# Kernel optimization log

Hardware: AMD Instinct MI355X
Metric: run time of the kernel (lower is better)

The kernel has to match this reference:

```python
import jax, jax.numpy as jnp
import numpy as np

N, E = 50000, 1600000
D_IN, D_OUT = 256, 64
ALPHA = 0.2        # LeakyReLU slope used on attention logits (self.leakyrelu)
BT_SLOPE = 0.01    # F.leaky_relu default slope inside relu_bt


def _xavier_normal(key, shape, gain):
    fan_in, fan_out = shape[0], shape[1]
    std = gain * np.sqrt(2.0 / (fan_in + fan_out))
    return jax.random.normal(key, shape, dtype=jnp.float32) * std


def relu_bt(x):
    # -threshold(-leaky_relu(x), -t, -t) == min(leaky_relu(x), t), t = ||x||_inf (detached)
    t = jax.lax.stop_gradient(jnp.max(jnp.abs(x)))
    y = jnp.where(x >= 0, x, BT_SLOPE * x)
    return jnp.minimum(y, t)


def setup_inputs() -> dict:
    key = jax.random.key(0)
    k0, k1, k2, k3, k4, k5 = jax.random.split(key, 6)
    inp = jax.random.normal(k0, (N, D_IN), dtype=jnp.float32)
    edge = jax.random.randint(k1, (2, E), 0, N, dtype=jnp.int64)
    W_high = _xavier_normal(k2, (D_IN, D_OUT), 1.414)
    W_low = _xavier_normal(k3, (D_IN, D_OUT), 1.414)
    a_high = _xavier_normal(k4, (1, D_OUT), 1.414)
    a_low = _xavier_normal(k5, (1, D_OUT), 1.414)
    return {"input": inp, "edge": edge, "W_high": W_high, "W_low": W_low,
            "a_high": a_high, "a_low": a_low}


def reference(input, edge, W_high, W_low, a_high, a_low):
    n = input.shape[0]
    src, dst = edge[0], edge[1]

    h_high = relu_bt(input @ W_high)  # [N, D_OUT]
    h_low = relu_bt(input @ W_low)    # [N, D_OUT]

    # a @ (h[src] -/+ h[dst])^T == (a.h)[src] -/+ (a.h)[dst]: compute per-node scalar
    # projections first, then gather scalars per edge (avoids [E, D_OUT] edge features).
    s_high = h_high @ a_high[0]       # [N]
    s_low = h_low @ a_low[0]          # [N]

    def lrelu(x):
        return jnp.where(x >= 0, x, ALPHA * x)

    edge_e_high = jnp.exp(-lrelu(s_high[src] - s_high[dst]))  # [E]
    edge_e_low = jnp.exp(-lrelu(s_low[src] + s_low[dst]))     # [E]
    # dropout p=0.0 -> identity

    # sparse A @ ones -> per-row sum of attention weights
    rowsum_high = jax.ops.segment_sum(edge_e_high, src, num_segments=n)[:, None]
    rowsum_low = jax.ops.segment_sum(edge_e_low, src, num_segments=n)[:, None]

    # sparse A @ h -> weighted aggregation of neighbor features
    hp_high = jax.ops.segment_sum(edge_e_high[:, None] * h_high[dst], src, num_segments=n)
    hp_low = jax.ops.segment_sum(edge_e_low[:, None] * h_low[dst], src, num_segments=n)

    hp_high = hp_high / (rowsum_high + 1e-16)
    hp_low = hp_low / (rowsum_low + 1e-16)

    # concat=True branch
    return relu_bt(jnp.concatenate([hp_high, hp_low], axis=1))  # [N, 2*D_OUT]
```

## Files before the change

### kernel.cpp

```cpp
#include <hip/hip_runtime.h>
#include <hip/hip_bf16.h>
#include <cstdint>

#define NN    50000
#define NE    1600000
#define DIN   256
#define DOUT  64

#define BKT   196
#define BCAP  10240
#define EPB   4096
#define EPT   16
#define NBIN  391
#define MTB   64
#define NGEMM 782
#define NAGG  1568

typedef __attribute__((ext_vector_type(8))) short frag8;
typedef __attribute__((ext_vector_type(4))) float fragc;

union PK { __hip_bfloat162 b2; uint32_t u; };
union CH { frag8 v; uint32_t u[4]; };

__device__ __forceinline__ float leaky01(float x) { return x >= 0.f ? x : 0.01f * x; }

__device__ __forceinline__ uint32_t pk2(float lo, float hi) {
  PK p; p.b2 = __float22bfloat162_rn(make_float2(lo, hi)); return p.u;
}

__device__ __forceinline__ int   bcast_i(int v, int lane) {
  return __builtin_amdgcn_readlane(v, lane);
}

__device__ __forceinline__ float bfH(uint32_t u) { return __uint_as_float(u << 16); }
__device__ __forceinline__ float bfL(uint32_t u) { return __uint_as_float(u & 0xffff0000u); }

__global__ __launch_bounds__(256) void prep_kernel(
    const float* __restrict__ Wh, const float* __restrict__ Wl,
    __hip_bfloat16* __restrict__ Wt, int* __restrict__ cursor)
{
  if (blockIdx.x == 0 && threadIdx.x < 256) cursor[threadIdx.x] = 0;
  int g = blockIdx.x * 256 + threadIdx.x;
  if (g < 2 * DOUT * DIN) {
    int m = g >> 14, rem = g & 16383;
    int n = rem >> 8, k = rem & 255;
    float v = (m ? Wl : Wh)[k * DOUT + n];
    Wt[g] = __float2bfloat16(v);
  }
}

__global__ __launch_bounds__(256) void fused_kernel(
    const float* __restrict__ inp, const __hip_bfloat16* __restrict__ Wt,
    const float* __restrict__ ah, const float* __restrict__ al,
    const int* __restrict__ edge, int* __restrict__ cursor,
    uint32_t* __restrict__ binned, uint32_t* __restrict__ HL,
    float2* __restrict__ ss)
{
  __shared__ __align__(16) char smem[32768];

  const int idx = blockIdx.x;
  const int t = threadIdx.x;

  if (idx < NBIN) {
    uint32_t* stage = (uint32_t*)smem;
    int* hist4 = (int*)(smem + 16384);
    int* cur4  = (int*)(smem + 20480);
    int* histT = (int*)(smem + 24576);
    int* scn   = (int*)(smem + 25600);
    int* sexc  = (int*)(smem + 26624);
    int* bg    = (int*)(smem + 27648);

    const int w = t >> 6;
    const int e0 = idx * EPB;
    uint32_t v[EPT];
#pragma unroll
    for (int i = 0; i < EPT; i++) {
      int e = e0 + i * 256 + t;
      if (e < NE) {
        v[i] = ((uint32_t)edge[e] << 16) | (uint32_t)edge[NE + e];
      } else {
        v[i] = 0xFFFFFFFFu;
      }
    }
    hist4[t] = 0; hist4[256 + t] = 0; hist4[512 + t] = 0; hist4[768 + t] = 0;
    cur4[t]  = 0; cur4[256 + t]  = 0; cur4[512 + t]  = 0; cur4[768 + t]  = 0;
    __syncthreads();
#pragma unroll
    for (int i = 0; i < EPT; i++) {
      int b = v[i] >> 24;
      if (b < BKT) atomicAdd(&hist4[(w << 8) + b], 1);
    }
    __syncthreads();
    {
      int h0 = hist4[t], h1 = hist4[256 + t], h2 = hist4[512 + t], h3 = hist4[768 + t];
      hist4[t] = 0; hist4[256 + t] = h0; hist4[512 + t] = h0 + h1; hist4[768 + t] = h0 + h1 + h2;
      int hb = h0 + h1 + h2 + h3;
      histT[t] = hb;
      scn[t] = hb;
    }
    __syncthreads();
    for (int off = 1; off < 256; off <<= 1) {
      int vv = scn[t] + ((t >= off) ? scn[t - off] : 0);
      __syncthreads();
      scn[t] = vv;
      __syncthreads();
    }
    {
      sexc[t] = scn[t] - histT[t];
      bg[t] = histT[t] ? atomicAdd(&cursor[t], histT[t]) : 0;
    }
    __syncthreads();
#pragma unroll
    for (int i = 0; i < EPT; i++) {
      int b = v[i] >> 24;
      if (b < BKT) {
        int pos = atomicAdd(&cur4[(w << 8) + b], 1);
        stage[sexc[b] + hist4[(w << 8) + b] + pos] = v[i];
      }
    }
    __syncthreads();
    const int total = scn[255];
    for (int i = t; i < total; i += 256) {
      uint32_t vv = stage[i];
      int lo = vv >> 24;
      int ofs = bg[lo] + (i - sexc[lo]);
      if (ofs < BCAP) binned[(size_t)lo * BCAP + ofs] = vv;
    }
    return;
  }

  frag8* asmem = (frag8*)smem;
  const int gid = idx - NBIN;
  const int n0 = gid * MTB;
  const int lane = t & 63;
  const int w = t >> 6;
  const int quad = lane >> 4, nn = lane & 15;

  const float4* inp4 = (const float4*)inp;
#pragma unroll
  for (int i = 0; i < 8; i++) {
    int c = i * 256 + t;
    int r = c & 15;
    int cc = c >> 4;
    int qd = cc & 3;
    int wq = cc >> 2;
    int row = ((wq >> 3) << 4) + r;
    int k0 = ((wq & 7) << 5) + (qd << 3);
    int node = n0 + row;
    float4 a0 = make_float4(0.f, 0.f, 0.f, 0.f), a1 = a0;
    if (node < NN) {
      a0 = inp4[(size_t)node * 64 + (k0 >> 2)];
      a1 = inp4[(size_t)node * 64 + (k0 >> 2) + 1];
    }
    CH ch;
    ch.u[0] = pk2(a0.x, a0.y);
    ch.u[1] = pk2(a0.z, a0.w);
    ch.u[2] = pk2(a1.x, a1.y);
    ch.u[3] = pk2(a1.z, a1.w);
    asmem[c] = ch.v;
  }
  __syncthreads();

  fragc accH[4], accL[4];
#pragma unroll
  for (int c = 0; c < 4; c++) {
    accH[c] = (fragc){0.f, 0.f, 0.f, 0.f};
    accL[c] = (fragc){0.f, 0.f, 0.f, 0.f};
  }

  const frag8* Wt8 = (const frag8*)Wt;
#pragma unroll
  for (int q = 0; q < 8; q++) {
    frag8 af = asmem[(w << 9) + (q << 6) + lane];
#pragma unroll
    for (int c = 0; c < 4; c++) {
      frag8 bh = Wt8[(c * 16 + nn) * 32 + q * 4 + quad];
      frag8 bl = Wt8[(64 + c * 16 + nn) * 32 + q * 4 + quad];
      accH[c] = __builtin_amdgcn_mfma_f32_16x16x32_bf16(af, bh, accH[c], 0, 0, 0);
      accL[c] = __builtin_amdgcn_mfma_f32_16x16x32_bf16(af, bl, accL[c], 0, 0, 0);
    }
  }

  float ahv[4], alv[4];
#pragma unroll
  for (int c = 0; c < 4; c++) { ahv[c] = ah[c * 16 + nn]; alv[c] = al[c * 16 + nn]; }
#pragma unroll
  for (int r = 0; r < 4; r++) {
    int node = n0 + (w << 4) + (quad << 2) + r;
    float sH = 0.f, sL = 0.f;
#pragma unroll
    for (int c = 0; c < 4; c++) {
      float hH = leaky01(accH[c][r]);
      float hL = leaky01(accL[c][r]);
      if (node < NN) HL[(size_t)node * DOUT + c * 16 + nn] = pk2(hH, hL);
      sH += hH * ahv[c];
      sL += hL * alv[c];
    }
#pragma unroll
    for (int off = 1; off < 16; off <<= 1) {
      sH += __shfl_xor(sH, off);
      sL += __shfl_xor(sL, off);
    }
    if (nn == 0 && node < NN) ss[node] = make_float2(sH, sL);
  }
}

__global__ __launch_bounds__(1024) void csr_kernel(
    const uint32_t* __restrict__ binned, const int* __restrict__ cursor,
    const float2* __restrict__ ss, uint16_t* __restrict__ dstS,
    uint32_t* __restrict__ wS, uint32_t* __restrict__ rowinfo,
    float2* __restrict__ rs)
{
  __shared__ float2 ssl[256];
  __shared__ int cnt[256], cur[256], stt[256], scn[256];
  __shared__ float rsH[256], rsL[256];
  const int b = blockIdx.x;
  const int t = threadIdx.x;
  if (t < 256) {
    cnt[t] = 0; cur[t] = 0; rsH[t] = 0.f; rsL[t] = 0.f;
    int node = (b << 8) + t;
    ssl[t] = (node < NN) ? ss[node] : make_float2(0.f, 0.f);
  }
  __syncthreads();
  int nE = cursor[b]; if (nE > BCAP) nE = BCAP;
  const uint32_t* eb = binned + (size_t)b * BCAP;

  uint32_t v[10], wv[10];
#pragma unroll
  for (int i = 0; i < 10; i++) {
    int e = i * 1024 + t;
    v[i] = (e < nE) ? eb[e] : 0xFFFFFFFFu;
  }
#pragma unroll
  for (int i = 0; i < 10; i++) {
    if (v[i] != 0xFFFFFFFFu) {
      int loc = (v[i] >> 16) & 255;
      int dst = v[i] & 0xffff;
      float2 sd = ss[dst];
      float2 sl = ssl[loc];
      float xh = sl.x - sd.x;
      xh = (xh >= 0.f) ? xh : 0.2f * xh;
      float eh = __expf(-xh);
      float xl = sl.y + sd.y;
      xl = (xl >= 0.f) ? xl : 0.2f * xl;
      float el = __expf(-xl);
      wv[i] = pk2(eh, el);
      atomicAdd(&cnt[loc], 1);
      atomicAdd(&rsH[loc], eh);
      atomicAdd(&rsL[loc], el);
    }
  }
  __syncthreads();
  if (t < 256) scn[t] = cnt[t];
  __syncthreads();
  for (int off = 1; off < 256; off <<= 1) {
    int vv = 0;
    if (t < 256) vv = scn[t] + ((t >= off) ? scn[t - off] : 0);
    __syncthreads();
    if (t < 256) scn[t] = vv;
    __syncthreads();
  }
  if (t < 256) stt[t] = scn[t] - cnt[t];
  __syncthreads();
#pragma unroll
  for (int i = 0; i < 10; i++) {
    if (v[i] != 0xFFFFFFFFu) {
      int loc = (v[i] >> 16) & 255;
      int pos = atomicAdd(&cur[loc], 1);
      size_t o = (size_t)b * BCAP + stt[loc] + pos;
      dstS[o] = (uint16_t)(v[i] & 0xffff);
      wS[o] = wv[i];
    }
  }
  __syncthreads();
  if (t < 256) {
    int node = (b << 8) + t;
    if (node < NN) {
      int c = cnt[t]; if (c > 255) c = 255;
      rowinfo[node] = ((uint32_t)(b * BCAP + stt[t]) << 8) | (uint32_t)c;
      rs[node] = make_float2(rsH[t], rsL[t]);
    }
  }
}

__global__ __launch_bounds__(256) void agg_kernel(
    const uint16_t* __restrict__ dstS, const uint32_t* __restrict__ wS,
    const uint32_t* __restrict__ rowinfo, const float2* __restrict__ rs,
    const uint32_t* __restrict__ HL, float* __restrict__ out)
{
  const int t = threadIdx.x;
  const int w = t >> 6, lane = t & 63;
  const int node0 = blockIdx.x * 32 + w * 8;

  for (int i = 0; i < 8; i++) {
    int node = node0 + i;
    if (node >= NN) continue;
    uint32_t ri = rowinfo[node];
    int d = ri & 255;
    size_t ofs = ri >> 8;
    float2 rsv = rs[node];

    float accH = 0.f, accL = 0.f;
    for (int base = 0; base < d; base += 64) {
      int m = d - base; if (m > 64) m = 64;
      int dst_l = 0, w_l = 0;
      if (lane < m) {
        dst_l = dstS[ofs + base + lane];
        w_l   = (int)wS[ofs + base + lane];
      }
      int j = 0;
      for (; j + 8 <= m; j += 8) {
        uint32_t u[8]; uint32_t ww[8];
#pragma unroll
        for (int x = 0; x < 8; x++) {
          int dd = bcast_i(dst_l, j + x);
          ww[x] = (uint32_t)bcast_i(w_l, j + x);
          u[x]  = HL[((uint32_t)dd << 6) + lane];
        }
#pragma unroll
        for (int x = 0; x < 8; x++) {
          accH += bfH(ww[x]) * bfH(u[x]);
          accL += bfL(ww[x]) * bfL(u[x]);
        }
      }
      for (; j < m; j++) {
        int dd = bcast_i(dst_l, j);
        uint32_t wwx = (uint32_t)bcast_i(w_l, j);
        uint32_t u = HL[((uint32_t)dd << 6) + lane];
        accH += bfH(wwx) * bfH(u);
        accL += bfL(wwx) * bfL(u);
      }
    }

    float oh = accH / (rsv.x + 1e-16f);
    float ol = accL / (rsv.y + 1e-16f);
    out[(size_t)node * 128 + lane]      = leaky01(oh);
    out[(size_t)node * 128 + 64 + lane] = leaky01(ol);
  }
}

extern "C" void kernel_launch(void* const* d_in, const int* in_sizes, int n_in,
                              void* d_out, int out_size, void* d_ws, size_t ws_size,
                              hipStream_t stream) {
  const float* inp  = (const float*)d_in[0];
  const int*   edge = (const int*)d_in[1];
  const float* Wh   = (const float*)d_in[2];
  const float* Wl   = (const float*)d_in[3];
  const float* ah   = (const float*)d_in[4];
  const float* al   = (const float*)d_in[5];
  float* out = (float*)d_out;

  char* ws = (char*)d_ws;
  uint32_t* HL      = (uint32_t*)(ws + 0);
  float2*   ss      = (float2*)  (ws + 12800000);
  uint32_t* binned  = (uint32_t*)(ws + 13200000);
  int*      cursor  = (int*)     (ws + 21228160);
  __hip_bfloat16* Wt = (__hip_bfloat16*)(ws + 21229184);
  uint32_t* wS      = (uint32_t*)(ws + 21294720);
  uint16_t* dstS    = (uint16_t*)(ws + 29322880);
  uint32_t* rowinfo = (uint32_t*)(ws + 33336960);
  float2*   rs      = (float2*)  (ws + 33536960);

  prep_kernel<<<128, 256, 0, stream>>>(Wh, Wl, Wt, cursor);
  fused_kernel<<<NBIN + NGEMM, 256, 0, stream>>>(inp, Wt, ah, al, edge,
                                                 cursor, binned, HL, ss);
  csr_kernel<<<BKT, 1024, 0, stream>>>(binned, cursor, ss, dstS, wS, rowinfo, rs);
  agg_kernel<<<NAGG, 256, 0, stream>>>(dstS, wS, rowinfo, rs, HL, out);
}
```

Baseline: 237.3 us.

## Fuse CSR build into aggregation kernel using shared-memory per-half-bucket edge lists

```diff
diff --git a/kernel.cpp b/kernel.cpp
--- a/kernel.cpp
+++ b/kernel.cpp
@@ -14,7 +14,7 @@
 #define NBIN  391
 #define MTB   64
 #define NGEMM 782
-#define NAGG  1568
+#define ACAP  4608
 
 typedef __attribute__((ext_vector_type(8))) short frag8;
 typedef __attribute__((ext_vector_type(4))) float fragc;
@@ -205,108 +205,85 @@
   }
 }
 
-__global__ __launch_bounds__(1024) void csr_kernel(
+__global__ __launch_bounds__(512) void agg_kernel(
     const uint32_t* __restrict__ binned, const int* __restrict__ cursor,
-    const float2* __restrict__ ss, uint16_t* __restrict__ dstS,
-    uint32_t* __restrict__ wS, uint32_t* __restrict__ rowinfo,
-    float2* __restrict__ rs)
+    const float2* __restrict__ ss, const uint32_t* __restrict__ HL,
+    float* __restrict__ out)
 {
-  __shared__ float2 ssl[256];
-  __shared__ int cnt[256], cur[256], stt[256], scn[256];
-  __shared__ float rsH[256], rsL[256];
-  const int b = blockIdx.x;
+  __shared__ uint16_t dstL[ACAP];
+  __shared__ uint32_t wL[ACAP];
+  __shared__ int cnt[128], cur[128], scn[128], stt[128];
+  __shared__ float rsH[128], rsL[128];
+  __shared__ float2 ssl[128];
+
+  const int b = blockIdx.x >> 1, half = blockIdx.x & 1;
   const int t = threadIdx.x;
-  if (t < 256) {
+  const int n0 = (b << 8) + (half << 7);
+
+  if (t < 128) {
     cnt[t] = 0; cur[t] = 0; rsH[t] = 0.f; rsL[t] = 0.f;
-    int node = (b << 8) + t;
+    int node = n0 + t;
     ssl[t] = (node < NN) ? ss[node] : make_float2(0.f, 0.f);
   }
   __syncthreads();
   int nE = cursor[b]; if (nE > BCAP) nE = BCAP;
   const uint32_t* eb = binned + (size_t)b * BCAP;
 
-  uint32_t v[10], wv[10];
-#pragma unroll
-  for (int i = 0; i < 10; i++) {
-    int e = i * 1024 + t;
-    v[i] = (e < nE) ? eb[e] : 0xFFFFFFFFu;
-  }
-#pragma unroll
-  for (int i = 0; i < 10; i++) {
-    if (v[i] != 0xFFFFFFFFu) {
-      int loc = (v[i] >> 16) & 255;
-      int dst = v[i] & 0xffff;
+  for (int i = t; i < nE; i += 512) {
+    uint32_t v = eb[i];
+    int loc = (v >> 16) & 255;
+    if ((loc >> 7) == half) atomicAdd(&cnt[loc & 127], 1);
+  }
+  __syncthreads();
+  if (t < 128) scn[t] = cnt[t];
+  __syncthreads();
+  for (int off = 1; off < 128; off <<= 1) {
+    int vv = 0;
+    if (t < 128) vv = scn[t] + ((t >= off) ? scn[t - off] : 0);
+    __syncthreads();
+    if (t < 128) scn[t] = vv;
+    __syncthreads();
+  }
+  if (t < 128) stt[t] = scn[t] - cnt[t];
+  __syncthreads();
+
+  for (int i = t; i < nE; i += 512) {
+    uint32_t v = eb[i];
+    int loc = (v >> 16) & 255;
+    if ((loc >> 7) == half) {
+      int l = loc & 127;
+      int dst = v & 0xffff;
       float2 sd = ss[dst];
-      float2 sl = ssl[loc];
-      float xh = sl.x - sd.x;
-      xh = (xh >= 0.f) ? xh : 0.2f * xh;
+      float2 sl = ssl[l];
+      float xh = sl.x - sd.x; xh = (xh >= 0.f) ? xh : 0.2f * xh;
       float eh = __expf(-xh);
-      float xl = sl.y + sd.y;
-      xl = (xl >= 0.f) ? xl : 0.2f * xl;
+      float xl = sl.y + sd.y; xl = (xl >= 0.f) ? xl : 0.2f * xl;
       float el = __expf(-xl);
-      wv[i] = pk2(eh, el);
-      atomicAdd(&cnt[loc], 1);
-      atomicAdd(&rsH[loc], eh);
-      atomicAdd(&rsL[loc], el);
-    }
-  }
-  __syncthreads();
-  if (t < 256) scn[t] = cnt[t];
-  __syncthreads();
-  for (int off = 1; off < 256; off <<= 1) {
-    int vv = 0;
-    if (t < 256) vv = scn[t] + ((t >= off) ? scn[t - off] : 0);
-    __syncthreads();
-    if (t < 256) scn[t] = vv;
-    __syncthreads();
-  }
-  if (t < 256) stt[t] = scn[t] - cnt[t];
-  __syncthreads();
-#pragma unroll
-  for (int i = 0; i < 10; i++) {
-    if (v[i] != 0xFFFFFFFFu) {
-      int loc = (v[i] >> 16) & 255;
-      int pos = atomicAdd(&cur[loc], 1);
-      size_t o = (size_t)b * BCAP + stt[loc] + pos;
-      dstS[o] = (uint16_t)(v[i] & 0xffff);
-      wS[o] = wv[i];
-    }
-  }
-  __syncthreads();
-  if (t < 256) {
-    int node = (b << 8) + t;
-    if (node < NN) {
-      int c = cnt[t]; if (c > 255) c = 255;
-      rowinfo[node] = ((uint32_t)(b * BCAP + stt[t]) << 8) | (uint32_t)c;
-      rs[node] = make_float2(rsH[t], rsL[t]);
-    }
-  }
-}
-
-__global__ __launch_bounds__(256) void agg_kernel(
-    const uint16_t* __restrict__ dstS, const uint32_t* __restrict__ wS,
-    const uint32_t* __restrict__ rowinfo, const float2* __restrict__ rs,
-    const uint32_t* __restrict__ HL, float* __restrict__ out)
-{
-  const int t = threadIdx.x;
+      atomicAdd(&rsH[l], eh);
+      atomicAdd(&rsL[l], el);
+      int pos = atomicAdd(&cur[l], 1);
+      int o = stt[l] + pos;
+      if (o < ACAP) { dstL[o] = (uint16_t)dst; wL[o] = pk2(eh, el); }
+    }
+  }
+  __syncthreads();
+
   const int w = t >> 6, lane = t & 63;
-  const int node0 = blockIdx.x * 32 + w * 8;
-
-  for (int i = 0; i < 8; i++) {
-    int node = node0 + i;
+  for (int i = 0; i < 16; i++) {
+    int l = (w << 4) + i;
+    int node = n0 + l;
     if (node >= NN) continue;
-    uint32_t ri = rowinfo[node];
-    int d = ri & 255;
-    size_t ofs = ri >> 8;
-    float2 rsv = rs[node];
+    int d = cnt[l], st = stt[l];
+    if (st + d > ACAP) d = ACAP - st;
+    if (d < 0) d = 0;
 
     float accH = 0.f, accL = 0.f;
     for (int base = 0; base < d; base += 64) {
       int m = d - base; if (m > 64) m = 64;
       int dst_l = 0, w_l = 0;
       if (lane < m) {
-        dst_l = dstS[ofs + base + lane];
-        w_l   = (int)wS[ofs + base + lane];
+        dst_l = dstL[st + base + lane];
+        w_l   = (int)wL[st + base + lane];
       }
       int j = 0;
       for (; j + 8 <= m; j += 8) {
@@ -332,8 +309,8 @@
       }
     }
 
-    float oh = accH / (rsv.x + 1e-16f);
-    float ol = accL / (rsv.y + 1e-16f);
+    float oh = accH / (rsH[l] + 1e-16f);
+    float ol = accL / (rsL[l] + 1e-16f);
     out[(size_t)node * 128 + lane]      = leaky01(oh);
     out[(size_t)node * 128 + 64 + lane] = leaky01(ol);
   }
@@ -356,14 +333,9 @@
   uint32_t* binned  = (uint32_t*)(ws + 13200000);
   int*      cursor  = (int*)     (ws + 21228160);
   __hip_bfloat16* Wt = (__hip_bfloat16*)(ws + 21229184);
-  uint32_t* wS      = (uint32_t*)(ws + 21294720);
-  uint16_t* dstS    = (uint16_t*)(ws + 29322880);
-  uint32_t* rowinfo = (uint32_t*)(ws + 33336960);
-  float2*   rs      = (float2*)  (ws + 33536960);
 
   prep_kernel<<<128, 256, 0, stream>>>(Wh, Wl, Wt, cursor);
   fused_kernel<<<NBIN + NGEMM, 256, 0, stream>>>(inp, Wt, ah, al, edge,
                                                  cursor, binned, HL, ss);
-  csr_kernel<<<BKT, 1024, 0, stream>>>(binned, cursor, ss, dstS, wS, rowinfo, rs);
-  agg_kernel<<<NAGG, 256, 0, stream>>>(dstS, wS, rowinfo, rs, HL, out);
-}
+  agg_kernel<<<BKT * 2, 512, 0, stream>>>(binned, cursor, ss, HL, out);
+}
```

New measurement: 240.9 us. No clear change (+1.5%).
